# Kernel optimization log

Measured on AMD Instinct MI355X. Metric: run time of the kernel, lower is better.

Reference implementation:

```python
import jax, jax.numpy as jnp
import numpy as np

NC, NW, E, EW = 100000, 500, 600000, 25000
H, L, DFF, CF, WF = 128, 3, 512, 32, 16


def setup_inputs() -> dict:
    key = jax.random.key(0)
    ks = iter(jax.random.split(key, 48))
    def nrm(shape, s=0.05):
        return jax.random.normal(next(ks), shape, jnp.float32) * s
    inp = {}
    inp["cell_x"] = jax.random.normal(next(ks), (NC, CF), jnp.float32)
    inp["well_x"] = jax.random.normal(next(ks), (NW, WF), jnp.float32)
    inp["c2c_edge_index"] = jax.random.randint(next(ks), (2, E), 0, NC)
    inp["c2c_edge_attr"] = jax.random.normal(next(ks), (E, 1), jnp.float32)
    inp["c2w_src"] = jax.random.randint(next(ks), (EW,), 0, NC)
    inp["c2w_dst"] = jax.random.randint(next(ks), (EW,), 0, NW)
    inp["W_cell"] = nrm((CF, H)); inp["b_cell"] = jnp.zeros((H,), jnp.float32)
    inp["W_well"] = nrm((WF, H)); inp["b_well"] = jnp.zeros((H,), jnp.float32)
    inp["W_ee"] = nrm((1, H));   inp["b_ee"] = jnp.zeros((H,), jnp.float32)
    inp["gW"]  = nrm((L, H, H))
    inp["gas"] = nrm((L, H)); inp["gad"] = nrm((L, H)); inp["gae"] = nrm((L, H))
    inp["gWe"] = nrm((L, H, H)); inp["gb"] = jnp.zeros((L, H), jnp.float32)
    inp["n1g"] = jnp.ones((L, H), jnp.float32); inp["n1b"] = jnp.zeros((L, H), jnp.float32)
    inp["fW1"] = nrm((L, H, DFF)); inp["fb1"] = jnp.zeros((L, DFF), jnp.float32)
    inp["fW2"] = nrm((L, DFF, H)); inp["fb2"] = jnp.zeros((L, H), jnp.float32)
    inp["n2g"] = jnp.ones((L, H), jnp.float32); inp["n2b"] = jnp.zeros((L, H), jnp.float32)
    inp["wW"] = nrm((H, H)); inp["was"] = nrm((H,)); inp["wad"] = nrm((H,))
    inp["wb"] = jnp.zeros((H,), jnp.float32)
    inp["mW1"] = nrm((H, H)); inp["mb1"] = jnp.zeros((H,), jnp.float32)
    inp["mW2"] = nrm((H, 75)); inp["mb2"] = jnp.zeros((75,), jnp.float32)
    return inp


def _layer_norm(x, g, b):
    mu = x.mean(-1, keepdims=True)
    v = ((x - mu) ** 2).mean(-1, keepdims=True)
    return (x - mu) * jax.lax.rsqrt(v + 1e-5) * g + b


def _seg_softmax(a, seg, n):
    # numerically stable softmax over edges grouped by destination node
    m = jax.ops.segment_max(a, seg, num_segments=n)
    e = jnp.exp(a - m[seg])
    s = jax.ops.segment_sum(e, seg, num_segments=n)
    s = jnp.where(s == 0, 1.0, s)
    return e / s[seg]


def reference(cell_x, well_x, c2c_edge_index, c2c_edge_attr, c2w_src, c2w_dst,
              W_cell, b_cell, W_well, b_well, W_ee, b_ee,
              gW, gas, gad, gae, gWe, gb,
              n1g, n1b, fW1, fb1, fW2, fb2, n2g, n2b,
              wW, was, wad, wb, mW1, mb1, mW2, mb2):
    src, dst = c2c_edge_index[0], c2c_edge_index[1]
    h = cell_x @ W_cell + b_cell           # [NC, H]
    hw = well_x @ W_well + b_well          # [NW, H]
    ea = c2c_edge_attr @ W_ee + b_ee       # [E, H] embedded edge features
    for i in range(L):
        # GATConv with edge features (heads=1, concat=False, no self loops)
        xn = _layer_norm(h, n1g[i], n1b[i])
        hs = xn @ gW[i]                    # [NC, H]
        alpha = (hs @ gas[i])[src] + (hs @ gad[i])[dst] + (ea @ gWe[i]) @ gae[i]
        alpha = jax.nn.leaky_relu(alpha, 0.2)
        alpha = _seg_softmax(alpha, dst, NC)
        msg = jax.ops.segment_sum(hs[src] * alpha[:, None], dst, num_segments=NC) + gb[i]
        h = h + msg                        # residual (dropout = identity in eval)
        xn = _layer_norm(h, n2g[i], n2b[i])
        h = h + (jax.nn.relu(xn @ fW1[i] + fb1[i]) @ fW2[i] + fb2[i])
    # cell -> well bipartite GATConv (shared lin for src/dst, no edge feats)
    hc = h @ wW                            # [NC, H]
    hwp = hw @ wW                          # [NW, H]
    a = (hc @ was)[c2w_src] + (hwp @ wad)[c2w_dst]
    a = jax.nn.leaky_relu(a, 0.2)
    a = _seg_softmax(a, c2w_dst, NW)
    h_well = jax.ops.segment_sum(hc[c2w_src] * a[:, None], c2w_dst, num_segments=NW) + wb
    out = jax.nn.relu(h_well @ mW1 + mb1) @ mW2 + mb2
    return out.reshape(-1, 3, 25)
```

## Files before the change

### kernel.cpp

```cpp
#include <hip/hip_runtime.h>
#include <hip/hip_bf16.h>

#define NC 100000
#define NW 500
#define NE_CC 600000
#define NE_CW 25000
#define H 128
#define NL 3
#define DFF 512
#define DC 64

typedef __bf16 bf16x8 __attribute__((ext_vector_type(8)));
typedef float f32x4 __attribute__((ext_vector_type(4)));
#define MFMA16(a,b,c) __builtin_amdgcn_mfma_f32_16x16x32_bf16(a,b,c,0,0,0)

__device__ __forceinline__ float wsum(float v){
  #pragma unroll
  for (int o = 32; o; o >>= 1) v += __shfl_xor(v, o, 64);
  return v;
}
__device__ __forceinline__ float gsum16(float v){
  #pragma unroll
  for (int o = 1; o < 16; o <<= 1) v += __shfl_xor(v, o, 64);
  return v;
// ... 34 lines not shown
        __float2bfloat16(v);
  }
}
__global__ void prep_imgW2_k(const float* __restrict__ in, char* __restrict__ img){
  int tot = 3 * 65536;
  for (int i = blockIdx.x * 256 + threadIdx.x; i < tot; i += gridDim.x * 256){
    int j = i & 7, lane = (i >> 3) & 63, f = (i >> 9) & 15, ch = (i >> 13) & 7, l = i >> 16;
    int lr = lane & 15, lk = lane >> 4;
    int ks = f >> 3, nt = f & 7;
    int k = ch * 64 + ks * 32 + lk * 8 + j, n = nt * 16 + lr;
    float v = in[(size_t)l * 65536 + (size_t)k * 128 + n];
    *(__hip_bfloat16*)(img + (size_t)(l * 8 + ch) * 16384 + f * 1024 + lane * 16 + j * 2) =
        __float2bfloat16(v);
  }
}

__global__ __launch_bounds__(256) void embed_ln_k(const float* __restrict__ x,
    const float* __restrict__ W, const float* __restrict__ b,
    const float* __restrict__ g, const float* __restrict__ lb,
    float* __restrict__ h, __hip_bfloat16* __restrict__ xn, int M)
{
  int lane = threadIdx.x & 63, wid = threadIdx.x >> 6;
  float w0[32], w1[32];
  #pragma unroll
  for (int k = 0; k < 32; k++){
    w0[k] = W[k * 128 + lane];
    w1[k] = W[k * 128 + 64 + lane];
  }
  float b0 = b[lane], b1 = b[lane + 64];
  float g0 = g[lane], g1 = g[lane + 64];
  float e0 = lb[lane], e1 = lb[lane + 64];
  for (int n = blockIdx.x * 4 + wid; n < M; n += gridDim.x * 4){
    const float4* xr = (const float4*)(x + (size_t)n * 32);
    float xs[32];
    #pragma unroll
    for (int q = 0; q < 8; q++){
      float4 t = xr[q];
      xs[4*q] = t.x; xs[4*q+1] = t.y; xs[4*q+2] = t.z; xs[4*q+3] = t.w;
    }
    float a0 = b0, a1 = b1;
    #pragma unroll
    for (int k = 0; k < 32; k++){ a0 += xs[k] * w0[k]; a1 += xs[k] * w1[k]; }
    h[(size_t)n * H + lane]      = a0;
    h[(size_t)n * H + lane + 64] = a1;
    float mu = wsum(a0 + a1) * (1.f / 128.f);
    float d0 = a0 - mu, d1 = a1 - mu;
    float var = wsum(d0 * d0 + d1 * d1) * (1.f / 128.f);
    float rs = rsqrtf(var + 1e-5f);
    xn[(size_t)n * H + lane]      = __float2bfloat16(d0 * rs * g0 + e0);
    xn[(size_t)n * H + lane + 64] = __float2bfloat16(d1 * rs * g1 + e1);
  }
}

template<int K>
__global__ __launch_bounds__(256) void embed_k(const float* __restrict__ x,
    const float* __restrict__ W, const float* __restrict__ b,
    float* __restrict__ h, int M)
{
  __shared__ float sW[K * 128];
  for (int t = threadIdx.x; t < K * 128; t += 256) sW[t] = W[t];
  __syncthreads();
  int j = threadIdx.x & 127, half = threadIdx.x >> 7;
  float bj = b[j];
  for (int n = blockIdx.x * 2 + half; n < M; n += gridDim.x * 2){
    const float* xr = x + (size_t)n * K;
    float acc = bj;
    #pragma unroll
    for (int k = 0; k < K; k++) acc += xr[k] * sW[k * 128 + j];
    h[(size_t)n * H + j] = acc;
  }
}

__global__ void coeff_k(const float* __restrict__ gWe, const float* __restrict__ gae,
    const float* __restrict__ Wee, const float* __restrict__ bee, float* __restrict__ coeff)
{
  __shared__ float red[4];
  int t = threadIdx.x;
  for (int i = 0; i < NL; i++){
    const float* Wr = gWe + ((size_t)i * H + t) * H;
    const float* ga = gae + (size_t)i * H;
    float w = 0.f;
    for (int k = 0; k < H; k++) w += Wr[k] * ga[k];
    float pc = Wee[t] * w, pd = bee[t] * w;
    pc = wsum(pc); pd = wsum(pd);
    if ((t & 63) == 0){ red[(t >> 6) * 2 + 0] = pc; red[(t >> 6) * 2 + 1] = pd; }
    __syncthreads();
    if (t == 0){ coeff[i] = red[0] + red[2]; coeff[NL + i] = red[1] + red[3]; }
    __syncthreads();
  }
}

__global__ __launch_bounds__(256) void dot2_k(const float* __restrict__ X,
    const float* __restrict__ va, float* __restrict__ oa, int M)
{
  int lane = threadIdx.x & 63, wid = threadIdx.x >> 6;
  int n = blockIdx.x * 4 + wid;
  if (n >= M) return;
  const float* row = X + (size_t)n * H;
  float a = wsum(row[lane] * va[lane] + row[lane + 64] * va[lane + 64]);
  if (lane == 0) oa[n] = a;
}

__global__ __launch_bounds__(512, 4) void gemm_mfma_k(
    const __hip_bfloat16* __restrict__ A, const char* __restrict__ Wimg,
    __hip_bfloat16* __restrict__ Cbf,
    const float* __restrict__ va, const float* __restrict__ vb,
    float* __restrict__ oa, float* __restrict__ ob, int M)
{
  __shared__ uint4 sW4[2048];
  char* sW = (char*)sW4;
  const int tid = threadIdx.x;
  const int lane = tid & 63, w = tid >> 6;
  const int n0 = blockIdx.x * 128;
  const int rw = w * 16;
  const int lr = lane & 15, lk = lane >> 4;

  {
    int go = w * 1024 + lane * 16;
    #pragma unroll
    for (int q = 0; q < 4; q++)
      gload16(Wimg + q * 8192 + go, sW + q * 8192 + w * 1024);
  }

  const int arow = n0 + rw + lr;
  bf16x8 aX[4];
  if (arow < M){
    #pragma unroll
    for (int ks = 0; ks < 4; ks++)
      aX[ks] = *(const bf16x8*)(A + (size_t)arow * 128 + ks * 32 + lk * 8);
  } else {
    #pragma unroll
    for (int ks = 0; ks < 4; ks++) aX[ks] = (bf16x8){0,0,0,0,0,0,0,0};
  }
  __syncthreads();

  f32x4 acc[8];
  #pragma unroll
  for (int i = 0; i < 8; i++) acc[i] = (f32x4){0.f, 0.f, 0.f, 0.f};
  #pragma unroll
  for (int ks = 0; ks < 4; ks++){
    #pragma unroll
    for (int nt = 0; nt < 8; nt++){
      bf16x8 b = *(const bf16x8*)(sW + ((ks << 3) + nt) * 1024 + (lane << 4));
      acc[nt] = MFMA16(aX[ks], b, acc[nt]);
    }
  }
  #pragma unroll
  for (int nt = 0; nt < 8; nt++){
    int col = nt * 16 + lr;
    #pragma unroll
    for (int r = 0; r < 4; r++){
      int row = n0 + rw + lk * 4 + r;
      if (row < M) Cbf[(size_t)row * 128 + col] = __float2bfloat16(acc[nt][r]);
    }
  }
  {
    float vac[8], vbc[8];
    #pragma unroll
    for (int nt = 0; nt < 8; nt++){
      vac[nt] = va[nt * 16 + lr];
      vbc[nt] = vb ? vb[nt * 16 + lr] : 0.f;
    }
    #pragma unroll
    for (int r = 0; r < 4; r++){
      float da = 0.f, db = 0.f;
      #pragma unroll
      for (int nt = 0; nt < 8; nt++){
        da += acc[nt][r] * vac[nt];
        db += acc[nt][r] * vbc[nt];
      }
      #pragma unroll
      for (int o = 1; o < 16; o <<= 1){
        da += __shfl_xor(da, o, 64);
        db += __shfl_xor(db, o, 64);
      }
      int row = n0 + rw + lk * 4 + r;
      if (lr == 0 && row < M){
        oa[row] = da;
        if (ob) ob[row] = db;
      }
    }
  }
}

__global__ __launch_bounds__(512, 4) void mega_k(
    const int* __restrict__ incl, const int* __restrict__ csr,
    const int* __restrict__ src, const float* __restrict__ attr,
    const float* __restrict__ coeff, int ci,
    const float* __restrict__ as_in, const float* __restrict__ ad_in,
    const __hip_bfloat16* __restrict__ X,
    const float* __restrict__ gbv,
    const float* __restrict__ n2gv, const float* __restrict__ n2bv,
    float* __restrict__ h,
    const char* __restrict__ W1img, const float* __restrict__ b1,
    const char* __restrict__ W2img, const float* __restrict__ b2,
    const float* __restrict__ lng, const float* __restrict__ lnb,
    const char* __restrict__ Wg,
    const float* __restrict__ va, const float* __restrict__ vb,
    float* __restrict__ oa, float* __restrict__ ob,
    __hip_bfloat16* __restrict__ Cbf, int mode, int M)
{
  __shared__ uint4 sW1_4[2][1024];
  __shared__ uint4 sW2_4[2][1024];
  __shared__ uint4 sT4[1024];
  char* sT = (char*)sT4;
  const int tid = threadIdx.x;
  const int lane = tid & 63, w = tid >> 6;
  const int n0 = blockIdx.x * 128;
  const int rw = w * 16;
  const int lr = lane & 15, lk = lane >> 4;
  const int gl = lane & 15, grp = lane >> 4;
  const int go = w * 1024 + lane * 16;
  const int lo = w * 1024;
  char* sTw = sT + w * 2048;
  char* aimgW = (w < 4) ? ((char*)sW1_4[1] + w * 4096)
                        : ((char*)sW2_4[1] + (w - 4) * 4096);

  gload16(W1img + go,        (char*)sW1_4[0] + lo);
  gload16(W1img + 8192 + go, (char*)sW1_4[0] + 8192 + lo);
  gload16(W2img + go,        (char*)sW2_4[0] + lo);
  gload16(W2img + 8192 + go, (char*)sW2_4[0] + 8192 + lo);

  const float c0 = coeff[ci], c1 = coeff[NL + ci];
  const int gbase = grp << 4;
  const int nb = n0 + w * 16 + grp * 4;

#define GACC2(A, U, P) \
    A[0] += (P) * __uint_as_float((U).x << 16); \
    A[1] += (P) * __uint_as_float((U).x & 0xffff0000u); \
    A[2] += (P) * __uint_as_float((U).y << 16); \
    A[3] += (P) * __uint_as_float((U).y & 0xffff0000u); \
    A[4] += (P) * __uint_as_float((U).z << 16); \
    A[5] += (P) * __uint_as_float((U).z & 0xffff0000u); \
    A[6] += (P) * __uint_as_float((U).w << 16); \
    A[7] += (P) * __uint_as_float((U).w & 0xffff0000u);

#define NODE_EPI(Q, ACC) { \
    int n = nb + (Q); \
    char* adst = aimgW + ((gl >> 2) << 10) + ((((gl & 3) << 4) + grp * 4 + (Q)) << 4); \
    if (n >= M){ *(uint4*)adst = make_uint4(0u,0u,0u,0u); } else { \
      float inv = (s4[Q] == 0.f) ? 0.f : 1.f / s4[Q]; \
      int j0 = gl * 8; \
      float4 h0 = *(float4*)&h[(size_t)n * H + j0]; \
      float4 h1 = *(float4*)&h[(size_t)n * H + j0 + 4]; \
      float4 g0 = *(const float4*)&gbv[j0]; \
      float4 g1 = *(const float4*)&gbv[j0 + 4]; \
      float hv[8]; \
      hv[0] = h0.x + ACC[0]*inv + g0.x; hv[1] = h0.y + ACC[1]*inv + g0.y; \
      hv[2] = h0.z + ACC[2]*inv + g0.z; hv[3] = h0.w + ACC[3]*inv + g0.w; \
      hv[4] = h1.x + ACC[4]*inv + g1.x; hv[5] = h1.y + ACC[5]*inv + g1.y; \
      hv[6] = h1.z + ACC[6]*inv + g1.z; hv[7] = h1.w + ACC[7]*inv + g1.w; \
      float ls = 0.f; \
      _Pragma("unroll") for (int i = 0; i < 8; i++) ls += hv[i]; \
      float mu = gsum16(ls) * (1.f / H); \
      float vs = 0.f; \
      _Pragma("unroll") for (int i = 0; i < 8; i++){ float d = hv[i]-mu; vs += d*d; } \
      float var = gsum16(vs) * (1.f / H); \
      float rsq = rsqrtf(var + 1e-5f); \
      float4 o0, o1; \
      o0.x=hv[0]; o0.y=hv[1]; o0.z=hv[2]; o0.w=hv[3]; \
      o1.x=hv[4]; o1.y=hv[5]; o1.z=hv[6]; o1.w=hv[7]; \
      *(float4*)&h[(size_t)n * H + j0] = o0; \
      *(float4*)&h[(size_t)n * H + j0 + 4] = o1; \
      float4 gg0 = *(const float4*)&n2gv[j0]; \
      float4 gg1 = *(const float4*)&n2gv[j0 + 4]; \
      float4 bb0 = *(const float4*)&n2bv[j0]; \
      float4 bb1 = *(const float4*)&n2bv[j0 + 4]; \
      float xo[8]; \
      xo[0]=(hv[0]-mu)*rsq*gg0.x+bb0.x; xo[1]=(hv[1]-mu)*rsq*gg0.y+bb0.y; \
      xo[2]=(hv[2]-mu)*rsq*gg0.z+bb0.z; xo[3]=(hv[3]-mu)*rsq*gg0.w+bb0.w; \
      xo[4]=(hv[4]-mu)*rsq*gg1.x+bb1.x; xo[5]=(hv[5]-mu)*rsq*gg1.y+bb1.y; \
      xo[6]=(hv[6]-mu)*rsq*gg1.z+bb1.z; xo[7]=(hv[7]-mu)*rsq*gg1.w+bb1.w; \
      uint4 ow; unsigned* owp = (unsigned*)&ow; \
      _Pragma("unroll") for (int i = 0; i < 4; i++){ \
// ... 73 lines not shown
    for (int q = 0; q < 4; q++){
      int n = nb + q;
      char* adst = aimgW + ((gl >> 2) << 10) + ((((gl & 3) << 4) + grp * 4 + q) << 4);
      if (n >= M){ *(uint4*)adst = make_uint4(0u,0u,0u,0u); continue; }
      int beg = beg4[q];
      int end = beg4[q] + cnt4[q];
      float adn = ad_in[n];
      float m = -1e30f, s = 0.f;
      float acc[8];
      #pragma unroll
      for (int i = 0; i < 8; i++) acc[i] = 0.f;
      for (int base = beg; base < end; base += 16){
        int idx = base + gl;
        bool valid = idx < end;
        int e = valid ? csr[idx] : 0;
        int sv = valid ? src[e] : 0;
        float a = -1e30f;
        if (valid){
          a = as_in[sv] + adn + attr[e] * c0 + c1;
          a = (a > 0.f) ? a : 0.2f * a;
        }
        float cmx = gmax16(a);
        float nm = fmaxf(m, cmx);
        float sc = expf(m - nm);
        #pragma unroll
        for (int i = 0; i < 8; i++) acc[i] *= sc;
        s *= sc;
        float p = valid ? expf(a - nm) : 0.f;
        s += gsum16(p);
        m = nm;
        int cnt = min(16, end - base);
        for (int t = 0; t < cnt; t++){
          float pt = __shfl(p, gbase + t, 64);
          int st = __shfl(sv, gbase + t, 64);
          uint4 u = *(const uint4*)(X + (size_t)st * H + gl * 8);
          GACC2(acc, u, pt)
        }
      }
      float s4q = s;
      float s4[4]; s4[q] = s4q;
      NODE_EPI(q, acc)
    }
  }
#undef GACC2

  asm volatile("s_waitcnt lgkmcnt(0)" ::: "memory");
  bf16x8 aX[4];
  #pragma unroll
  for (int ks = 0; ks < 4; ks++)
    aX[ks] = *(const bf16x8*)(aimgW + (ks << 10) + (lane << 4));
  asm volatile("s_waitcnt lgkmcnt(0) vmcnt(0)" ::: "memory");
  __builtin_amdgcn_s_barrier();

  f32x4 acc2[8];
  #pragma unroll
  for (int i = 0; i < 8; i++) acc2[i] = (f32x4){0.f, 0.f, 0.f, 0.f};

  const int rdA = ((lane ^ ((lane >> 3) & 7)) << 4);

  for (int ch = 0; ch < DFF / DC; ch++){
    const int cur = ch & 1;
    if (ch < DFF / DC - 1){
      const char* g1 = W1img + (size_t)(ch + 1) * 16384;
      const char* g2 = W2img + (size_t)(ch + 1) * 16384;
      char* d1 = (char*)sW1_4[cur ^ 1];
      char* d2 = (char*)sW2_4[cur ^ 1];
      gload16(g1 + go,        d1 + lo);
      gload16(g1 + 8192 + go, d1 + 8192 + lo);
      gload16(g2 + go,        d2 + lo);
      gload16(g2 + 8192 + go, d2 + 8192 + lo);
    } else {
      gload16(Wg + go,         (char*)sW1_4[0] + lo);
      gload16(Wg + 8192 + go,  (char*)sW1_4[0] + 8192 + lo);
      gload16(Wg + 16384 + go, (char*)sW2_4[0] + lo);
      gload16(Wg + 24576 + go, (char*)sW2_4[0] + 8192 + lo);
    }

    const char* W1c = (const char*)sW1_4[cur];
    const char* W2c = (const char*)sW2_4[cur];

    f32x4 acc1[4];
    #pragma unroll
    for (int i = 0; i < 4; i++) acc1[i] = (f32x4){0.f, 0.f, 0.f, 0.f};
    #pragma unroll
    for (int ks = 0; ks < 4; ks++){
      #pragma unroll
      for (int nt = 0; nt < 4; nt++){
        bf16x8 b = *(const bf16x8*)(W1c + ((ks << 2) + nt) * 1024 + (lane << 4));
        acc1[nt] = MFMA16(aX[ks], b, acc1[nt]);
      }
    }
    #pragma unroll
    for (int nt = 0; nt < 4; nt++){
      int col = nt * 16 + lr;
      float bb = b1[ch * DC + col];
      int ksp = col >> 5;
      int qhi = ((col >> 3) & 3) << 4;
      int jb  = (col & 7) << 1;
      #pragma unroll
      for (int r = 0; r < 4; r++){
        int slot = qhi + lk * 4 + r;
        int slotp = slot ^ ((slot >> 3) & 7);
        float v = fmaxf(acc1[nt][r] + bb, 0.f);
        *(__hip_bfloat16*)(sTw + (ksp << 10) + (slotp << 4) + jb) = __float2bfloat16(v);
      }
    }
    asm volatile("s_waitcnt lgkmcnt(0)" ::: "memory");

    #pragma unroll
    for (int ks = 0; ks < 2; ks++){
      bf16x8 a = *(const bf16x8*)(sTw + (ks << 10) + rdA);
      #pragma unroll
      for (int nt = 0; nt < 8; nt++){
        bf16x8 b = *(const bf16x8*)(W2c + ((ks << 3) + nt) * 1024 + (lane << 4));
        acc2[nt] = MFMA16(a, b, acc2[nt]);
      }
    }
    if (ch < DFF / DC - 1){
      asm volatile("s_waitcnt vmcnt(0)" ::: "memory");
      __builtin_amdgcn_s_barrier();
    }
  }

  asm volatile("s_waitcnt vmcnt(0)" ::: "memory");
  __builtin_amdgcn_s_barrier();

  float b2c[8];
  #pragma unroll
  for (int nt = 0; nt < 8; nt++) b2c[nt] = b2[nt * 16 + lr];
  float lngc[8], lnbc[8];
  if (mode == 0){
    #pragma unroll
    for (int nt = 0; nt < 8; nt++){
      lngc[nt] = lng[nt * 16 + lr];
      lnbc[nt] = lnb[nt * 16 + lr];
    }
  }

  #pragma unroll
  for (int r = 0; r < 4; r++){
    int row = n0 + rw + lk * 4 + r;
    bool ok = row < M;
    float val[8]; float sum = 0.f;
    #pragma unroll
    for (int nt = 0; nt < 8; nt++){
      int col = nt * 16 + lr;
      float hv = ok ? h[(size_t)row * 128 + col] : 0.f;
      val[nt] = hv + acc2[nt][r] + b2c[nt];
      sum += val[nt];
    }
    float mu = 0.f, rs = 1.f;
    if (mode == 0){
      #pragma unroll
      for (int o = 1; o < 16; o <<= 1) sum += __shfl_xor(sum, o, 64);
      mu = sum * (1.f / 128.f);
      float vs = 0.f;
      #pragma unroll
      for (int nt = 0; nt < 8; nt++){ float d = val[nt] - mu; vs += d * d; }
      #pragma unroll
      for (int o = 1; o < 16; o <<= 1) vs += __shfl_xor(vs, o, 64);
      rs = rsqrtf(vs * (1.f / 128.f) + 1e-5f);
    }
    #pragma unroll
    for (int nt = 0; nt < 8; nt++){
      int col = nt * 16 + lr;
      if (mode == 0 && ok) h[(size_t)row * 128 + col] = val[nt];
      float xo = (mode == 0) ? ((val[nt] - mu) * rs * lngc[nt] + lnbc[nt]) : val[nt];
      int lanep = ((((nt & 1) << 1) + (lr >> 3)) << 4) + (lk << 2) + r;
      *(__hip_bfloat16*)(aimgW + ((nt >> 1) << 10) + (lanep << 4) + ((lr & 7) << 1)) =
          __float2bfloat16(xo);
    }
  }
  asm volatile("s_waitcnt lgkmcnt(0)" ::: "memory");

  bf16x8 aG[4];
  #pragma unroll
  for (int ks = 0; ks < 4; ks++)
    aG[ks] = *(const bf16x8*)(aimgW + (ks << 10) + (lane << 4));
  f32x4 accG[8];
  #pragma unroll
  for (int i = 0; i < 8; i++) accG[i] = (f32x4){0.f, 0.f, 0.f, 0.f};
  #pragma unroll
  for (int ks = 0; ks < 4; ks++){
    #pragma unroll
    for (int nt = 0; nt < 8; nt++){
      const char* bptr = (ks < 2)
          ? ((const char*)sW1_4[0] + (((ks << 3) + nt) << 10) + (lane << 4))
          : ((const char*)sW2_4[0] + ((((ks - 2) << 3) + nt) << 10) + (lane << 4));
      accG[nt] = MFMA16(aG[ks], *(const bf16x8*)bptr, accG[nt]);
    }
  }
  #pragma unroll
  for (int nt = 0; nt < 8; nt++){
    int col = nt * 16 + lr;
    #pragma unroll
    for (int r = 0; r < 4; r++){
      int row = n0 + rw + lk * 4 + r;
      if (row < M) Cbf[(size_t)row * 128 + col] = __float2bfloat16(accG[nt][r]);
    }
  }
  {
    float vac[8], vbc[8];
    #pragma unroll
    for (int nt = 0; nt < 8; nt++){
      vac[nt] = va[nt * 16 + lr];
      vbc[nt] = vb ? vb[nt * 16 + lr] : 0.f;
    }
    #pragma unroll
    for (int r = 0; r < 4; r++){
      float da = 0.f, db = 0.f;
      #pragma unroll
      for (int nt = 0; nt < 8; nt++){
        da += accG[nt][r] * vac[nt];
        db += accG[nt][r] * vbc[nt];
      }
      #pragma unroll
      for (int o = 1; o < 16; o <<= 1){
        da += __shfl_xor(da, o, 64);
        db += __shfl_xor(db, o, 64);
      }
      int row = n0 + rw + lk * 4 + r;
      if (lr == 0 && row < M){
        oa[row] = da;
        if (ob) ob[row] = db;
      }
    }
  }
#undef NODE_EPI
}

__global__ __launch_bounds__(256) void gemm128_k(const float* __restrict__ A,
    const float* __restrict__ Bm, float* __restrict__ C, int M)
{
  __shared__ float sB[32 * 128];
  __shared__ float sA[64 * 33];
  const int tid = threadIdx.x;
  const int n0 = blockIdx.x * 64;
  const int j4 = (tid & 31) * 4;
  const int rB = (tid >> 5) * 8;
  float acc[8][4];
  #pragma unroll
  for (int r = 0; r < 8; r++){ acc[r][0]=acc[r][1]=acc[r][2]=acc[r][3]=0.f; }
  for (int kc = 0; kc < 128; kc += 32){
    for (int t = tid; t < 4096; t += 256){
      int kk = t >> 7, j = t & 127;
      sB[kk * 128 + j] = Bm[(size_t)(kc + kk) * H + j];
    }
    for (int t = tid; t < 2048; t += 256){
      int n = t >> 5, kk = t & 31; int row = n0 + n;
      sA[n * 33 + kk] = (row < M) ? A[(size_t)row * H + kc + kk] : 0.f;
    }
    __syncthreads();
    #pragma unroll 8
    for (int kk = 0; kk < 32; kk++){
      float4 bv = *(const float4*)&sB[kk * 128 + j4];
      #pragma unroll
      for (int r = 0; r < 8; r++){
        float av = sA[(rB + r) * 33 + kk];
        acc[r][0] += av * bv.x; acc[r][1] += av * bv.y;
        acc[r][2] += av * bv.z; acc[r][3] += av * bv.w;
      }
    }
    __syncthreads();
  }
  #pragma unroll
  for (int r = 0; r < 8; r++){
    int row = n0 + rB + r;
    if (row < M){
      float4 o; o.x = acc[r][0]; o.y = acc[r][1]; o.z = acc[r][2]; o.w = acc[r][3];
      *(float4*)&C[(size_t)row * H + j4] = o;
    }
  }
}

__global__ void count_k(const int* __restrict__ dst, int* __restrict__ cnt, int NE){
  int e = blockIdx.x * 256 + threadIdx.x;
  if (e < NE) atomicAdd(&cnt[dst[e]], 1);
}
__global__ void scan1_k(const int* __restrict__ in, int* __restrict__ out,
                        int* __restrict__ bsum, int N){
  __shared__ int sd[256];
  int tid = threadIdx.x;
  int base = blockIdx.x * 1024 + tid * 4;
  int v0 = (base + 0 < N) ? in[base + 0] : 0;
  int v1 = (base + 1 < N) ? in[base + 1] : 0;
  int v2 = (base + 2 < N) ? in[base + 2] : 0;
  int v3 = (base + 3 < N) ? in[base + 3] : 0;
  sd[tid] = v0 + v1 + v2 + v3;
  __syncthreads();
  for (int off = 1; off < 256; off <<= 1){
    int t = (tid >= off) ? sd[tid - off] : 0;
    __syncthreads();
    sd[tid] += t;
    __syncthreads();
  }
  int run = (tid > 0) ? sd[tid - 1] : 0;
  run += v0; if (base + 0 < N) out[base + 0] = run;
  run += v1; if (base + 1 < N) out[base + 1] = run;
  run += v2; if (base + 2 < N) out[base + 2] = run;
  run += v3; if (base + 3 < N) out[base + 3] = run;
  if (tid == 255) bsum[blockIdx.x] = sd[255];
}
__global__ void scan2_k(int* __restrict__ bs, int NB){
  __shared__ int sd[256];
  int tid = threadIdx.x;
  int base = tid * 4;
  int v0 = (base + 0 < NB) ? bs[base + 0] : 0;
  int v1 = (base + 1 < NB) ? bs[base + 1] : 0;
  int v2 = (base + 2 < NB) ? bs[base + 2] : 0;
  int v3 = (base + 3 < NB) ? bs[base + 3] : 0;
  sd[tid] = v0 + v1 + v2 + v3;
  __syncthreads();
  for (int off = 1; off < 256; off <<= 1){
    int t = (tid >= off) ? sd[tid - off] : 0;
    __syncthreads();
    sd[tid] += t;
    __syncthreads();
  }
  int run = (tid > 0) ? sd[tid - 1] : 0;
  run += v0; if (base + 0 < NB) bs[base + 0] = run;
  run += v1; if (base + 1 < NB) bs[base + 1] = run;
  run += v2; if (base + 2 < NB) bs[base + 2] = run;
  run += v3; if (base + 3 < NB) bs[base + 3] = run;
}
__global__ void scan3_k(int* __restrict__ out, const int* __restrict__ bsum, int N){
  int b = blockIdx.x;
  if (b == 0) return;
  int add = bsum[b - 1];
  int i = b * 1024 + threadIdx.x * 4;
  #pragma unroll
  for (int j = 0; j < 4; j++) if (i + j < N) out[i + j] += add;
}
__global__ void initfill_k(const int* __restrict__ incl, int* __restrict__ fill, int N){
  int i = blockIdx.x * 256 + threadIdx.x;
  if (i < N) fill[i] = (i == 0) ? 0 : incl[i - 1];
}
__global__ void fill_k(const int* __restrict__ dst, int* __restrict__ fill,
                       int* __restrict__ csr, int NE){
  int e = blockIdx.x * 256 + threadIdx.x;
  if (e < NE){
    int p = atomicAdd(&fill[dst[e]], 1);
    csr[p] = e;
  }
}

__global__ __launch_bounds__(256) void gat_k(
    const int* __restrict__ incl, const int* __restrict__ csr,
    const int* __restrict__ src,
    const float* __restrict__ as_, const float* __restrict__ ad_,
    const __hip_bfloat16* __restrict__ X, float* __restrict__ hout, int M)
{
  int lane = threadIdx.x & 63, wid = threadIdx.x >> 6;
  int grp = lane >> 4, gl = lane & 15;
  int n = blockIdx.x * 16 + wid * 4 + grp;
  if (n >= M) return;
  int beg = (n == 0) ? 0 : incl[n - 1];
  int end = incl[n];
  float adn = ad_[n];
  const int gbase = grp << 4;
  float m = -1e30f, s = 0.f;
  float acc[8];
  #pragma unroll
  for (int i = 0; i < 8; i++) acc[i] = 0.f;
#define GACC(U, P) \
    acc[0] += (P) * __uint_as_float((U).x << 16); \
    acc[1] += (P) * __uint_as_float((U).x & 0xffff0000u); \
    acc[2] += (P) * __uint_as_float((U).y << 16); \
    acc[3] += (P) * __uint_as_float((U).y & 0xffff0000u); \
    acc[4] += (P) * __uint_as_float((U).z << 16); \
    acc[5] += (P) * __uint_as_float((U).z & 0xffff0000u); \
    acc[6] += (P) * __uint_as_float((U).w << 16); \
    acc[7] += (P) * __uint_as_float((U).w & 0xffff0000u);
  for (int base = beg; base < end; base += 16){
    int idx = base + gl;
    bool valid = idx < end;
    int e = valid ? csr[idx] : 0;
    int sv = valid ? src[e] : 0;
    float a = -1e30f;
    if (valid){
      a = as_[sv] + adn;
      a = (a > 0.f) ? a : 0.2f * a;
    }
    float cm = gmax16(a);
    float nm = fmaxf(m, cm);
    float sc = expf(m - nm);
    #pragma unroll
    for (int i = 0; i < 8; i++) acc[i] *= sc;
    s *= sc;
    float p = valid ? expf(a - nm) : 0.f;
    s += gsum16(p);
    m = nm;
    int cnt = min(16, end - base);
    for (int t = 0; t < cnt; t++){
      float pt = __shfl(p, gbase + t, 64);
      int st = __shfl(sv, gbase + t, 64);
      uint4 u = *(const uint4*)(X + (size_t)st * H + gl * 8);
      GACC(u, pt)
    }
  }
#undef GACC
  float inv = (s == 0.f) ? 0.f : 1.f / s;
  int j0 = gl * 8;
  float4 o0, o1;
  o0.x = acc[0]*inv; o0.y = acc[1]*inv; o0.z = acc[2]*inv; o0.w = acc[3]*inv;
  o1.x = acc[4]*inv; o1.y = acc[5]*inv; o1.z = acc[6]*inv; o1.w = acc[7]*inv;
  *(float4*)&hout[(size_t)n * H + j0] = o0;
  *(float4*)&hout[(size_t)n * H + j0 + 4] = o1;
}

__global__ __launch_bounds__(128) void mlp_k(const float* __restrict__ hwell,
    const float* __restrict__ wb, const float* __restrict__ mW1,
// ... 21 lines not shown
{
  (void)in_sizes; (void)n_in; (void)out_size; (void)ws_size;
  const float* cell_x = (const float*)d_in[0];
  const float* well_x = (const float*)d_in[1];
  const int*   eidx   = (const int*)d_in[2];
  const float* eattr  = (const float*)d_in[3];
  const int*   wsrc   = (const int*)d_in[4];
  const int*   wdst   = (const int*)d_in[5];
  const float* W_cell = (const float*)d_in[6];
  const float* b_cell = (const float*)d_in[7];
  const float* W_well = (const float*)d_in[8];
  const float* b_well = (const float*)d_in[9];
  const float* W_ee   = (const float*)d_in[10];
  const float* b_ee   = (const float*)d_in[11];
  const float* gW     = (const float*)d_in[12];
  const float* gas    = (const float*)d_in[13];
  const float* gad    = (const float*)d_in[14];
  const float* gae    = (const float*)d_in[15];
  const float* gWe    = (const float*)d_in[16];
  const float* gb     = (const float*)d_in[17];
  const float* n1g    = (const float*)d_in[18];
  const float* n1b    = (const float*)d_in[19];
  const float* fW1    = (const float*)d_in[20];
  const float* fb1    = (const float*)d_in[21];
  const float* fW2    = (const float*)d_in[22];
  const float* fb2    = (const float*)d_in[23];
  const float* n2g    = (const float*)d_in[24];
  const float* n2b    = (const float*)d_in[25];
  const float* wW     = (const float*)d_in[26];
  const float* was    = (const float*)d_in[27];
  const float* wad    = (const float*)d_in[28];
  const float* wb     = (const float*)d_in[29];
  const float* mW1    = (const float*)d_in[30];
  const float* mb1    = (const float*)d_in[31];
  const float* mW2    = (const float*)d_in[32];
  const float* mb2    = (const float*)d_in[33];

  const int* src = eidx;
  const int* dst = eidx + NE_CC;

  char* wsb = (char*)d_ws;
  size_t off = 0;
  auto alloc = [&](size_t bytes) -> void* {
    void* p = wsb + off; off += (bytes + 255) & ~(size_t)255; return p;
  };
  float* h      = (float*)alloc((size_t)NC * H * 4);
  __hip_bfloat16* xnbf  = (__hip_bfloat16*)alloc((size_t)NC * H * 2);
  __hip_bfloat16* hsbf0 = (__hip_bfloat16*)alloc((size_t)NC * H * 2);
  __hip_bfloat16* hsbf1 = (__hip_bfloat16*)alloc((size_t)NC * H * 2);
  float* as0    = (float*)alloc((size_t)NC * 4);
  float* ad0    = (float*)alloc((size_t)NC * 4);
  float* as1    = (float*)alloc((size_t)NC * 4);
  float* ad1    = (float*)alloc((size_t)NC * 4);
  float* hw     = (float*)alloc((size_t)NW * H * 4);
  float* hwp    = (float*)alloc((size_t)NW * H * 4);
  float* hwell  = (float*)alloc((size_t)NW * H * 4);
  float* coeff  = (float*)alloc(64);
  char* gWimg = (char*)alloc((size_t)NL * 32768);
  char* wWimg = (char*)alloc(32768);
  char* W1img = (char*)alloc((size_t)NL * 131072);
  char* W2img = (char*)alloc((size_t)NL * 131072);
  int* cntC  = (int*)alloc((size_t)NC * 4);
  int* inclC = (int*)alloc((size_t)NC * 4);
  int* fillC = (int*)alloc((size_t)NC * 4);
  int* csrC  = (int*)alloc((size_t)NE_CC * 4);
  int* inclW = (int*)alloc((size_t)NW * 4);
  int* fillW = (int*)alloc((size_t)NW * 4);
  int* csrW  = (int*)alloc((size_t)NE_CW * 4);
  int* bsum  = (int*)alloc(1024 * 4);

  const int eBlocks  = (NE_CC + 255) / 256;
  const int ewBlocks = (NE_CW + 255) / 256;
  const int NBC = (NC + 1023) / 1024;
  const int NBW = (NW + 1023) / 1024;

  hipMemsetAsync(cntC, 0, (size_t)NC * 4, stream);
  count_k<<<eBlocks, 256, 0, stream>>>(dst, cntC, NE_CC);
  scan1_k<<<NBC, 256, 0, stream>>>(cntC, inclC, bsum, NC);
  scan2_k<<<1, 256, 0, stream>>>(bsum, NBC);
  scan3_k<<<NBC, 256, 0, stream>>>(inclC, bsum, NC);
  initfill_k<<<(NC + 255) / 256, 256, 0, stream>>>(inclC, fillC, NC);
  fill_k<<<eBlocks, 256, 0, stream>>>(dst, fillC, csrC, NE_CC);
  hipMemsetAsync(fillW, 0, (size_t)NW * 4, stream);
  count_k<<<ewBlocks, 256, 0, stream>>>(wdst, fillW, NE_CW);
  scan1_k<<<NBW, 256, 0, stream>>>(fillW, inclW, bsum, NW);
  scan2_k<<<1, 256, 0, stream>>>(bsum, NBW);
  scan3_k<<<NBW, 256, 0, stream>>>(inclW, bsum, NW);
  initfill_k<<<(NW + 255) / 256, 256, 0, stream>>>(inclW, fillW, NW);
  fill_k<<<ewBlocks, 256, 0, stream>>>(wdst, fillW, csrW, NE_CW);

  prep_imgGW_k<<<96, 256, 0, stream>>>(gW, gWimg, NL);
  prep_imgGW_k<<<32, 256, 0, stream>>>(wW, wWimg, 1);
  prep_imgW1_k<<<768, 256, 0, stream>>>(fW1, W1img);
  prep_imgW2_k<<<768, 256, 0, stream>>>(fW2, W2img);

  embed_ln_k<<<1024, 256, 0, stream>>>(cell_x, W_cell, b_cell, n1g, n1b, h, xnbf, NC);
  embed_k<16><<<250, 256, 0, stream>>>(well_x, W_well, b_well, hw, NW);
  coeff_k<<<1, 128, 0, stream>>>(gWe, gae, W_ee, b_ee, coeff);

  const int mfmaBlocks = (NC + 127) / 128;

  gemm_mfma_k<<<mfmaBlocks, 512, 0, stream>>>(xnbf, gWimg,
      hsbf0, gas, gad, as0, ad0, NC);

  for (int i = 0; i < NL; i++){
    const __hip_bfloat16* Xin = (i & 1) ? hsbf1 : hsbf0;
    __hip_bfloat16* Xout      = (i & 1) ? hsbf0 : hsbf1;
    const float* asi = (i & 1) ? as1 : as0;
    const float* adi = (i & 1) ? ad1 : ad0;
    float* aso = (i & 1) ? as0 : as1;
    float* ado = (i & 1) ? ad0 : ad1;
    if (i < NL - 1){
      mega_k<<<mfmaBlocks, 512, 0, stream>>>(inclC, csrC, src, eattr, coeff, i,
          asi, adi, Xin, gb + i * H, n2g + i * H, n2b + i * H, h,
          W1img + (size_t)i * 131072, fb1 + (size_t)i * DFF,
          W2img + (size_t)i * 131072, fb2 + (size_t)i * H,
          n1g + (i + 1) * H, n1b + (i + 1) * H,
          gWimg + (size_t)(i + 1) * 32768,
          gas + (i + 1) * H, gad + (i + 1) * H, aso, ado, Xout, 0, NC);
    } else {
      mega_k<<<mfmaBlocks, 512, 0, stream>>>(inclC, csrC, src, eattr, coeff, i,
          asi, adi, Xin, gb + i * H, n2g + i * H, n2b + i * H, h,
          W1img + (size_t)i * 131072, fb1 + (size_t)i * DFF,
          W2img + (size_t)i * 131072, fb2 + (size_t)i * H,
          n1g, n1b,
          wWimg, was, nullptr, aso, nullptr, Xout, 1, NC);
    }
  }

  gemm128_k<<<(NW + 63) / 64, 256, 0, stream>>>(hw, wW, hwp, NW);
  dot2_k<<<(NW + 3) / 4, 256, 0, stream>>>(hwp, wad, ad0, NW);
  gat_k<<<(NW + 15) / 16, 256, 0, stream>>>(inclW, csrW, wsrc,
      as1, ad0, hsbf1, hwell, NW);
  mlp_k<<<NW, 128, 0, stream>>>(hwell, wb, mW1, mb1, mW2, mb2, (float*)d_out);
}
```

Before: 584.6 us.

## Single-buffer FFN weight chunks in LDS to raise occupancy

```diff
diff --git a/kernel.cpp b/kernel.cpp
--- a/kernel.cpp
+++ b/kernel.cpp
@@ -241,7 +241,7 @@
   }
 }
 
-__global__ __launch_bounds__(512, 4) void mega_k(
+__global__ __launch_bounds__(512, 6) void mega_k(
     const int* __restrict__ incl, const int* __restrict__ csr,
     const int* __restrict__ src, const float* __restrict__ attr,
     const float* __restrict__ coeff, int ci,
@@ -258,8 +258,8 @@
     float* __restrict__ oa, float* __restrict__ ob,
     __hip_bfloat16* __restrict__ Cbf, int mode, int M)
 {
-  __shared__ uint4 sW1_4[2][1024];
-  __shared__ uint4 sW2_4[2][1024];
+  __shared__ uint4 sW1_4[1024];
+  __shared__ uint4 sW2_4[1024];
   __shared__ uint4 sT4[1024];
   char* sT = (char*)sT4;
   const int tid = threadIdx.x;
@@ -271,13 +271,8 @@
   const int go = w * 1024 + lane * 16;
   const int lo = w * 1024;
   char* sTw = sT + w * 2048;
-  char* aimgW = (w < 4) ? ((char*)sW1_4[1] + w * 4096)
-                        : ((char*)sW2_4[1] + (w - 4) * 4096);
-
-  gload16(W1img + go,        (char*)sW1_4[0] + lo);
-  gload16(W1img + 8192 + go, (char*)sW1_4[0] + 8192 + lo);
-  gload16(W2img + go,        (char*)sW2_4[0] + lo);
-  gload16(W2img + 8192 + go, (char*)sW2_4[0] + 8192 + lo);
+  char* aimgW = (w < 4) ? ((char*)sW1_4 + w * 4096)
+                        : ((char*)sW2_4 + (w - 4) * 4096);
 
   const float c0 = coeff[ci], c1 = coeff[NL + ci];
   const int gbase = grp << 4;
@@ -457,6 +452,13 @@
   asm volatile("s_waitcnt lgkmcnt(0) vmcnt(0)" ::: "memory");
   __builtin_amdgcn_s_barrier();
 
+  gload16(W1img + go,        (char*)sW1_4 + lo);
+  gload16(W1img + 8192 + go, (char*)sW1_4 + 8192 + lo);
+  gload16(W2img + go,        (char*)sW2_4 + lo);
+  gload16(W2img + 8192 + go, (char*)sW2_4 + 8192 + lo);
+  asm volatile("s_waitcnt vmcnt(0)" ::: "memory");
+  __builtin_amdgcn_s_barrier();
+
   f32x4 acc2[8];
   #pragma unroll
   for (int i = 0; i < 8; i++) acc2[i] = (f32x4){0.f, 0.f, 0.f, 0.f};
@@ -464,25 +466,8 @@
   const int rdA = ((lane ^ ((lane >> 3) & 7)) << 4);
 
   for (int ch = 0; ch < DFF / DC; ch++){
-    const int cur = ch & 1;
-    if (ch < DFF / DC - 1){
-      const char* g1 = W1img + (size_t)(ch + 1) * 16384;
-      const char* g2 = W2img + (size_t)(ch + 1) * 16384;
-      char* d1 = (char*)sW1_4[cur ^ 1];
-      char* d2 = (char*)sW2_4[cur ^ 1];
-      gload16(g1 + go,        d1 + lo);
-      gload16(g1 + 8192 + go, d1 + 8192 + lo);
-      gload16(g2 + go,        d2 + lo);
-      gload16(g2 + 8192 + go, d2 + 8192 + lo);
-    } else {
-      gload16(Wg + go,         (char*)sW1_4[0] + lo);
-      gload16(Wg + 8192 + go,  (char*)sW1_4[0] + 8192 + lo);
-      gload16(Wg + 16384 + go, (char*)sW2_4[0] + lo);
-      gload16(Wg + 24576 + go, (char*)sW2_4[0] + 8192 + lo);
-    }
-
-    const char* W1c = (const char*)sW1_4[cur];
-    const char* W2c = (const char*)sW2_4[cur];
+    const char* W1c = (const char*)sW1_4;
+    const char* W2c = (const char*)sW2_4;
 
     f32x4 acc1[4];
     #pragma unroll
@@ -522,13 +507,23 @@
       }
     }
     if (ch < DFF / DC - 1){
+      __builtin_amdgcn_s_barrier();
+      const char* g1 = W1img + (size_t)(ch + 1) * 16384;
+      const char* g2 = W2img + (size_t)(ch + 1) * 16384;
+      gload16(g1 + go,        (char*)sW1_4 + lo);
+      gload16(g1 + 8192 + go, (char*)sW1_4 + 8192 + lo);
+      gload16(g2 + go,        (char*)sW2_4 + lo);
+      gload16(g2 + 8192 + go, (char*)sW2_4 + 8192 + lo);
       asm volatile("s_waitcnt vmcnt(0)" ::: "memory");
       __builtin_amdgcn_s_barrier();
     }
   }
 
-  asm volatile("s_waitcnt vmcnt(0)" ::: "memory");
   __builtin_amdgcn_s_barrier();
+  gload16(Wg + go,         (char*)sW1_4 + lo);
+  gload16(Wg + 8192 + go,  (char*)sW1_4 + 8192 + lo);
+  gload16(Wg + 16384 + go, (char*)sW2_4 + lo);
+  gload16(Wg + 24576 + go, (char*)sW2_4 + 8192 + lo);
 
   float b2c[8];
   #pragma unroll
@@ -541,6 +536,8 @@
       lnbc[nt] = lnb[nt * 16 + lr];
     }
   }
+
+  unsigned xh01[4], xh23[4];
 
   #pragma unroll
   for (int r = 0; r < 4; r++){
@@ -566,35 +563,73 @@
       for (int o = 1; o < 16; o <<= 1) vs += __shfl_xor(vs, o, 64);
       rs = rsqrtf(vs * (1.f / 128.f) + 1e-5f);
     }
+    float xo8[8];
     #pragma unroll
     for (int nt = 0; nt < 8; nt++){
       int col = nt * 16 + lr;
       if (mode == 0 && ok) h[(size_t)row * 128 + col] = val[nt];
-      float xo = (mode == 0) ? ((val[nt] - mu) * rs * lngc[nt] + lnbc[nt]) : val[nt];
+      xo8[nt] = (mode == 0) ? ((val[nt] - mu) * rs * lngc[nt] + lnbc[nt]) : val[nt];
+    }
+    #pragma unroll
+    for (int nt = 0; nt < 4; nt++){
       int lanep = ((((nt & 1) << 1) + (lr >> 3)) << 4) + (lk << 2) + r;
-      *(__hip_bfloat16*)(aimgW + ((nt >> 1) << 10) + (lanep << 4) + ((lr & 7) << 1)) =
-          __float2bfloat16(xo);
+      *(__hip_bfloat16*)(sTw + ((nt >> 1) << 10) + (lanep << 4) + ((lr & 7) << 1)) =
+          __float2bfloat16(xo8[nt]);
+    }
+    {
+      __hip_bfloat16 a4 = __float2bfloat16(xo8[4]);
+      __hip_bfloat16 a5 = __float2bfloat16(xo8[5]);
+      __hip_bfloat16 a6 = __float2bfloat16(xo8[6]);
+      __hip_bfloat16 a7 = __float2bfloat16(xo8[7]);
+      xh01[r] = ((unsigned)(*(unsigned short*)&a5) << 16) | (*(unsigned short*)&a4);
+      xh23[r] = ((unsigned)(*(unsigned short*)&a7) << 16) | (*(unsigned short*)&a6);
     }
   }
   asm volatile("s_waitcnt lgkmcnt(0)" ::: "memory");
-
-  bf16x8 aG[4];
-  #pragma unroll
-  for (int ks = 0; ks < 4; ks++)
-    aG[ks] = *(const bf16x8*)(aimgW + (ks << 10) + (lane << 4));
+  bf16x8 aG0 = *(const bf16x8*)(sTw + (lane << 4));
+  bf16x8 aG1 = *(const bf16x8*)(sTw + 1024 + (lane << 4));
+  asm volatile("s_waitcnt lgkmcnt(0) vmcnt(0)" ::: "memory");
+  __builtin_amdgcn_s_barrier();
+
   f32x4 accG[8];
   #pragma unroll
   for (int i = 0; i < 8; i++) accG[i] = (f32x4){0.f, 0.f, 0.f, 0.f};
   #pragma unroll
-  for (int ks = 0; ks < 4; ks++){
-    #pragma unroll
-    for (int nt = 0; nt < 8; nt++){
-      const char* bptr = (ks < 2)
-          ? ((const char*)sW1_4[0] + (((ks << 3) + nt) << 10) + (lane << 4))
-          : ((const char*)sW2_4[0] + ((((ks - 2) << 3) + nt) << 10) + (lane << 4));
-      accG[nt] = MFMA16(aG[ks], *(const bf16x8*)bptr, accG[nt]);
-    }
-  }
+  for (int nt = 0; nt < 8; nt++){
+    bf16x8 b0 = *(const bf16x8*)((const char*)sW1_4 + (nt << 10) + (lane << 4));
+    accG[nt] = MFMA16(aG0, b0, accG[nt]);
+  }
+  #pragma unroll
+  for (int nt = 0; nt < 8; nt++){
+    bf16x8 b1v = *(const bf16x8*)((const char*)sW1_4 + ((8 + nt) << 10) + (lane << 4));
+    accG[nt] = MFMA16(aG1, b1v, accG[nt]);
+  }
+  #pragma unroll
+  for (int r = 0; r < 4; r++){
+    #pragma unroll
+    for (int i = 0; i < 4; i++){
+      int nt = 4 + i;
+      unsigned word = (i < 2) ? xh01[r] : xh23[r];
+      unsigned short bits = (unsigned short)((i & 1) ? (word >> 16) : (word & 0xffffu));
+      int lanep = ((((nt & 1) << 1) + (lr >> 3)) << 4) + (lk << 2) + r;
+      *(unsigned short*)(sTw + (((nt >> 1) & 1) << 10) + (lanep << 4) + ((lr & 7) << 1)) = bits;
+    }
+  }
+  asm volatile("s_waitcnt lgkmcnt(0)" ::: "memory");
+  bf16x8 aG2 = *(const bf16x8*)(sTw + (lane << 4));
+  bf16x8 aG3 = *(const bf16x8*)(sTw + 1024 + (lane << 4));
+  asm volatile("s_waitcnt lgkmcnt(0)" ::: "memory");
+  #pragma unroll
+  for (int nt = 0; nt < 8; nt++){
+    bf16x8 b2v = *(const bf16x8*)((const char*)sW2_4 + (nt << 10) + (lane << 4));
+    accG[nt] = MFMA16(aG2, b2v, accG[nt]);
+  }
+  #pragma unroll
+  for (int nt = 0; nt < 8; nt++){
+    bf16x8 b3 = *(const bf16x8*)((const char*)sW2_4 + ((8 + nt) << 10) + (lane << 4));
+    accG[nt] = MFMA16(aG3, b3, accG[nt]);
+  }
+
   #pragma unroll
   for (int nt = 0; nt < 8; nt++){
     int col = nt * 16 + lr;
```

Measured after the change: 704.8 us. 20.6% more time.

## Fold well attention into precomputed vector and merge small setup kernels

Applied to the files above, without the earlier changes.

```diff
diff --git a/kernel.cpp b/kernel.cpp
--- a/kernel.cpp
+++ b/kernel.cpp
@@ -110,31 +110,18 @@
   }
 }
 
-template<int K>
-__global__ __launch_bounds__(256) void embed_k(const float* __restrict__ x,
-    const float* __restrict__ W, const float* __restrict__ b,
-    float* __restrict__ h, int M)
-{
-  __shared__ float sW[K * 128];
-  for (int t = threadIdx.x; t < K * 128; t += 256) sW[t] = W[t];
-  __syncthreads();
-  int j = threadIdx.x & 127, half = threadIdx.x >> 7;
-  float bj = b[j];
-  for (int n = blockIdx.x * 2 + half; n < M; n += gridDim.x * 2){
-    const float* xr = x + (size_t)n * K;
-    float acc = bj;
-    #pragma unroll
-    for (int k = 0; k < K; k++) acc += xr[k] * sW[k * 128 + j];
-    h[(size_t)n * H + j] = acc;
-  }
-}
-
 __global__ void coeff_k(const float* __restrict__ gWe, const float* __restrict__ gae,
-    const float* __restrict__ Wee, const float* __restrict__ bee, float* __restrict__ coeff)
+    const float* __restrict__ Wee, const float* __restrict__ bee,
+    float* __restrict__ coeff,
+    const float* __restrict__ wW, const float* __restrict__ wad,
+    const float* __restrict__ Wwell, const float* __restrict__ bwell,
+    float* __restrict__ wvec)
 {
   __shared__ float red[4];
+  __shared__ float su[128];
   int t = threadIdx.x;
-  for (int i = 0; i < NL; i++){
+  int i = blockIdx.x;
+  if (i < NL){
     const float* Wr = gWe + ((size_t)i * H + t) * H;
     const float* ga = gae + (size_t)i * H;
     float w = 0.f;
@@ -144,19 +131,23 @@
     if ((t & 63) == 0){ red[(t >> 6) * 2 + 0] = pc; red[(t >> 6) * 2 + 1] = pd; }
     __syncthreads();
     if (t == 0){ coeff[i] = red[0] + red[2]; coeff[NL + i] = red[1] + red[3]; }
+  } else {
+    float u = 0.f;
+    const float* wWr = wW + (size_t)t * H;
+    for (int j = 0; j < H; j++) u += wWr[j] * wad[j];
+    su[t] = u;
     __syncthreads();
-  }
-}
-
-__global__ __launch_bounds__(256) void dot2_k(const float* __restrict__ X,
-    const float* __restrict__ va, float* __restrict__ oa, int M)
-{
-  int lane = threadIdx.x & 63, wid = threadIdx.x >> 6;
-  int n = blockIdx.x * 4 + wid;
-  if (n >= M) return;
-  const float* row = X + (size_t)n * H;
-  float a = wsum(row[lane] * va[lane] + row[lane + 64] * va[lane + 64]);
-  if (lane == 0) oa[n] = a;
+    if (t < 16){
+      float v = 0.f;
+      for (int k = 0; k < H; k++) v += Wwell[t * H + k] * su[k];
+      wvec[t] = v;
+    }
+    float pc = bwell[t] * su[t];
+    pc = wsum(pc);
+    if ((t & 63) == 0) red[t >> 6] = pc;
+    __syncthreads();
+    if (t == 0) wvec[16] = red[0] + red[1];
+  }
 }
 
 __global__ __launch_bounds__(512, 4) void gemm_mfma_k(
@@ -634,50 +625,6 @@
 #undef NODE_EPI
 }
 
-__global__ __launch_bounds__(256) void gemm128_k(const float* __restrict__ A,
-    const float* __restrict__ Bm, float* __restrict__ C, int M)
-{
-  __shared__ float sB[32 * 128];
-  __shared__ float sA[64 * 33];
-  const int tid = threadIdx.x;
-  const int n0 = blockIdx.x * 64;
-  const int j4 = (tid & 31) * 4;
-  const int rB = (tid >> 5) * 8;
-  float acc[8][4];
-  #pragma unroll
-  for (int r = 0; r < 8; r++){ acc[r][0]=acc[r][1]=acc[r][2]=acc[r][3]=0.f; }
-  for (int kc = 0; kc < 128; kc += 32){
-    for (int t = tid; t < 4096; t += 256){
-      int kk = t >> 7, j = t & 127;
-      sB[kk * 128 + j] = Bm[(size_t)(kc + kk) * H + j];
-    }
-    for (int t = tid; t < 2048; t += 256){
-      int n = t >> 5, kk = t & 31; int row = n0 + n;
-      sA[n * 33 + kk] = (row < M) ? A[(size_t)row * H + kc + kk] : 0.f;
-    }
-    __syncthreads();
-    #pragma unroll 8
-    for (int kk = 0; kk < 32; kk++){
-      float4 bv = *(const float4*)&sB[kk * 128 + j4];
-      #pragma unroll
-      for (int r = 0; r < 8; r++){
-        float av = sA[(rB + r) * 33 + kk];
-        acc[r][0] += av * bv.x; acc[r][1] += av * bv.y;
-        acc[r][2] += av * bv.z; acc[r][3] += av * bv.w;
-      }
-    }
-    __syncthreads();
-  }
-  #pragma unroll
-  for (int r = 0; r < 8; r++){
-    int row = n0 + rB + r;
-    if (row < M){
-      float4 o; o.x = acc[r][0]; o.y = acc[r][1]; o.z = acc[r][2]; o.w = acc[r][3];
-      *(float4*)&C[(size_t)row * H + j4] = o;
-    }
-  }
-}
-
 __global__ void count_k(const int* __restrict__ dst, int* __restrict__ cnt, int NE){
   int e = blockIdx.x * 256 + threadIdx.x;
   if (e < NE) atomicAdd(&cnt[dst[e]], 1);
@@ -728,17 +675,20 @@
   run += v2; if (base + 2 < NB) bs[base + 2] = run;
   run += v3; if (base + 3 < NB) bs[base + 3] = run;
 }
-__global__ void scan3_k(int* __restrict__ out, const int* __restrict__ bsum, int N){
+__global__ void scan3f_k(int* __restrict__ out, const int* __restrict__ bsum,
+                         int* __restrict__ fill, int N){
   int b = blockIdx.x;
-  if (b == 0) return;
-  int add = bsum[b - 1];
+  int add = (b == 0) ? 0 : bsum[b - 1];
   int i = b * 1024 + threadIdx.x * 4;
   #pragma unroll
-  for (int j = 0; j < 4; j++) if (i + j < N) out[i + j] += add;
-}
-__global__ void initfill_k(const int* __restrict__ incl, int* __restrict__ fill, int N){
-  int i = blockIdx.x * 256 + threadIdx.x;
-  if (i < N) fill[i] = (i == 0) ? 0 : incl[i - 1];
+  for (int j = 0; j < 4; j++){
+    if (i + j < N){
+      int v = out[i + j] + add;
+      if (b > 0) out[i + j] = v;
+      if (i + j + 1 < N) fill[i + j + 1] = v;
+    }
+  }
+  if (b == 0 && threadIdx.x == 0) fill[0] = 0;
 }
 __global__ void fill_k(const int* __restrict__ dst, int* __restrict__ fill,
                        int* __restrict__ csr, int NE){
@@ -749,10 +699,39 @@
   }
 }
 
+__global__ __launch_bounds__(1024) void csrw_k(const int* __restrict__ wdst,
+    int* __restrict__ inclW, int* __restrict__ csrW)
+{
+  __shared__ int cnt[512];
+  __shared__ int sc[512];
+  int t = threadIdx.x;
+  if (t < 512) cnt[t] = 0;
+  __syncthreads();
+  for (int e = t; e < NE_CW; e += 1024) atomicAdd(&cnt[wdst[e]], 1);
+  __syncthreads();
+  if (t < 512) sc[t] = cnt[t];
+  __syncthreads();
+  for (int off = 1; off < 512; off <<= 1){
+    int v = 0;
+    if (t < 512 && t >= off) v = sc[t - off];
+    __syncthreads();
+    if (t < 512) sc[t] += v;
+    __syncthreads();
+  }
+  if (t < NW) inclW[t] = sc[t];
+  if (t < 512) cnt[t] = (t == 0) ? 0 : sc[t - 1];
+  __syncthreads();
+  for (int e = t; e < NE_CW; e += 1024){
+    int p = atomicAdd(&cnt[wdst[e]], 1);
+    csrW[p] = e;
+  }
+}
+
 __global__ __launch_bounds__(256) void gat_k(
     const int* __restrict__ incl, const int* __restrict__ csr,
     const int* __restrict__ src,
-    const float* __restrict__ as_, const float* __restrict__ ad_,
+    const float* __restrict__ as_,
+    const float* __restrict__ wellx, const float* __restrict__ wv,
     const __hip_bfloat16* __restrict__ X, float* __restrict__ hout, int M)
 {
   int lane = threadIdx.x & 63, wid = threadIdx.x >> 6;
@@ -761,7 +740,7 @@
   if (n >= M) return;
   int beg = (n == 0) ? 0 : incl[n - 1];
   int end = incl[n];
-  float adn = ad_[n];
+  float adn = gsum16(wellx[(size_t)n * 16 + gl] * wv[gl]) + wv[16];
   const int gbase = grp << 4;
   float m = -1e30f, s = 0.f;
   float acc[8];
@@ -889,10 +868,9 @@
   float* ad0    = (float*)alloc((size_t)NC * 4);
   float* as1    = (float*)alloc((size_t)NC * 4);
   float* ad1    = (float*)alloc((size_t)NC * 4);
-  float* hw     = (float*)alloc((size_t)NW * H * 4);
-  float* hwp    = (float*)alloc((size_t)NW * H * 4);
   float* hwell  = (float*)alloc((size_t)NW * H * 4);
   float* coeff  = (float*)alloc(64);
+  float* wvec   = (float*)alloc(128);
   char* gWimg = (char*)alloc((size_t)NL * 32768);
   char* wWimg = (char*)alloc(32768);
   char* W1img = (char*)alloc((size_t)NL * 131072);
@@ -902,29 +880,19 @@
   int* fillC = (int*)alloc((size_t)NC * 4);
   int* csrC  = (int*)alloc((size_t)NE_CC * 4);
   int* inclW = (int*)alloc((size_t)NW * 4);
-  int* fillW = (int*)alloc((size_t)NW * 4);
   int* csrW  = (int*)alloc((size_t)NE_CW * 4);
   int* bsum  = (int*)alloc(1024 * 4);
 
-  const int eBlocks  = (NE_CC + 255) / 256;
-  const int ewBlocks = (NE_CW + 255) / 256;
+  const int eBlocks = (NE_CC + 255) / 256;
   const int NBC = (NC + 1023) / 1024;
-  const int NBW = (NW + 1023) / 1024;
 
   hipMemsetAsync(cntC, 0, (size_t)NC * 4, stream);
   count_k<<<eBlocks, 256, 0, stream>>>(dst, cntC, NE_CC);
   scan1_k<<<NBC, 256, 0, stream>>>(cntC, inclC, bsum, NC);
   scan2_k<<<1, 256, 0, stream>>>(bsum, NBC);
-  scan3_k<<<NBC, 256, 0, stream>>>(inclC, bsum, NC);
-  initfill_k<<<(NC + 255) / 256, 256, 0, stream>>>(inclC, fillC, NC);
+  scan3f_k<<<NBC, 256, 0, stream>>>(inclC, bsum, fillC, NC);
   fill_k<<<eBlocks, 256, 0, stream>>>(dst, fillC, csrC, NE_CC);
-  hipMemsetAsync(fillW, 0, (size_t)NW * 4, stream);
-  count_k<<<ewBlocks, 256, 0, stream>>>(wdst, fillW, NE_CW);
-  scan1_k<<<NBW, 256, 0, stream>>>(fillW, inclW, bsum, NW);
-  scan2_k<<<1, 256, 0, stream>>>(bsum, NBW);
-  scan3_k<<<NBW, 256, 0, stream>>>(inclW, bsum, NW);
-  initfill_k<<<(NW + 255) / 256, 256, 0, stream>>>(inclW, fillW, NW);
-  fill_k<<<ewBlocks, 256, 0, stream>>>(wdst, fillW, csrW, NE_CW);
+  csrw_k<<<1, 1024, 0, stream>>>(wdst, inclW, csrW);
 
   prep_imgGW_k<<<96, 256, 0, stream>>>(gW, gWimg, NL);
   prep_imgGW_k<<<32, 256, 0, stream>>>(wW, wWimg, 1);
@@ -932,8 +900,8 @@
   prep_imgW2_k<<<768, 256, 0, stream>>>(fW2, W2img);
 
   embed_ln_k<<<1024, 256, 0, stream>>>(cell_x, W_cell, b_cell, n1g, n1b, h, xnbf, NC);
-  embed_k<16><<<250, 256, 0, stream>>>(well_x, W_well, b_well, hw, NW);
-  coeff_k<<<1, 128, 0, stream>>>(gWe, gae, W_ee, b_ee, coeff);
+  coeff_k<<<4, 128, 0, stream>>>(gWe, gae, W_ee, b_ee, coeff,
+                                 wW, wad, W_well, b_well, wvec);
 
   const int mfmaBlocks = (NC + 127) / 128;
 
@@ -965,9 +933,7 @@
     }
   }
 
-  gemm128_k<<<(NW + 63) / 64, 256, 0, stream>>>(hw, wW, hwp, NW);
-  dot2_k<<<(NW + 3) / 4, 256, 0, stream>>>(hwp, wad, ad0, NW);
   gat_k<<<(NW + 15) / 16, 256, 0, stream>>>(inclW, csrW, wsrc,
-      as1, ad0, hsbf1, hwell, NW);
+      as1, well_x, wvec, hsbf1, hwell, NW);
   mlp_k<<<NW, 128, 0, stream>>>(hwell, wb, mW1, mb1, mW2, mb2, (float*)d_out);
 }
```

After: 539.2 us. -7.8%, faster.
